# Optimization experiments

Hardware: AMD Instinct MI355X
Metric: run time of the kernel (lower is better)

## Reference

```python
import jax, jax.numpy as jnp
import numpy as np

N, E, IN_DIM, OUT_DIM, HEADS = 50000, 800000, 128, 64, 2
NEG_SLOPE = 0.2  # DGL GATConv default leaky_relu slope


def setup_inputs() -> dict:
    key = jax.random.key(0)
    ks = jax.random.split(key, 11)
    p = lambda k, shape: jax.random.normal(k, shape, jnp.float32) * 0.05
    return dict(
        feature=jax.random.normal(ks[0], (N, IN_DIM), jnp.float32),
        src=jax.random.randint(ks[1], (E,), 0, N, jnp.int32),
        dst=jax.random.randint(ks[2], (E,), 0, N, jnp.int32),
        W1=p(ks[3], (IN_DIM, HEADS * OUT_DIM)),
        al1=p(ks[4], (HEADS, OUT_DIM)),
        ar1=p(ks[5], (HEADS, OUT_DIM)),
        b1=p(ks[6], (HEADS * OUT_DIM,)),
        W2=p(ks[7], (HEADS * OUT_DIM, OUT_DIM)),
        al2=p(ks[8], (1, OUT_DIM)),
        ar2=p(ks[9], (1, OUT_DIM)),
        b2=p(ks[10], (OUT_DIM,)),
    )


def gat_conv(x, W, al, ar, b, src, dst, n_nodes):
    # DGL GATConv (eval mode): fc -> per-node attn halves -> edge leaky_relu
    # -> edge-softmax grouped by dst -> scatter-weighted sum -> + bias
    H, D = al.shape
    h = (x @ W).reshape(n_nodes, H, D)               # [N,H,D]
    el = jnp.einsum('nhd,hd->nh', h, al)             # [N,H]
    er = jnp.einsum('nhd,hd->nh', h, ar)             # [N,H]
    e = jax.nn.leaky_relu(el[src] + er[dst], NEG_SLOPE)  # [E,H]
    m = jax.ops.segment_max(e, dst, num_segments=n_nodes)
    m = jnp.where(jnp.isfinite(m), m, 0.0)           # guard isolated dst nodes
    ex = jnp.exp(e - m[dst])                         # [E,H]
    s = jax.ops.segment_sum(ex, dst, num_segments=n_nodes)
    alpha = ex / s[dst]                              # edge-softmax weights
    out = jax.ops.segment_sum(alpha[:, :, None] * h[src], dst,
                              num_segments=n_nodes)  # [N,H,D]
    return out + b.reshape(H, D)


def reference(feature, src, dst, W1, al1, ar1, b1, W2, al2, ar2, b2):
    h1 = jax.nn.elu(gat_conv(feature, W1, al1, ar1, b1, src, dst, N))  # [N,2,D]
    h2 = gat_conv(h1.reshape(N, -1), W2, al2, ar2, b2, src, dst, N)    # [N,1,D]
    return (h1.mean(axis=1) + h2[:, 0, :]) * 0.5
```

## Files before the change

### kernel.cpp

```cpp
#include <hip/hip_runtime.h>
#include <hip/hip_fp16.h>
#include <math.h>

#define NNODES 50000
#define NEDGES 800000
#define CSR_STRIDE 48
#define NBUCKET 256
#define CHUNK 196
#define BCAP 4096
#define EPB 4096

typedef short bf16x8 __attribute__((ext_vector_type(8)));
typedef float f32x4  __attribute__((ext_vector_type(4)));

__device__ __forceinline__ unsigned bfpack(float a, float b) {
    unsigned ua = __float_as_uint(a), ub = __float_as_uint(b);
    ua = (ua + 0x7fffu + ((ua >> 16) & 1u)) >> 16;
    ub = (ub + 0x7fffu + ((ub >> 16) & 1u)) >> 16;
    return ua | (ub << 16);
}
__device__ __forceinline__ unsigned h2pack(float a, float b) {
    __half2 h = __floats2half2_rn(a, b);
    return *(unsigned*)&h;
}
__device__ __forceinline__ float hlo(unsigned u) {
    union { unsigned u; __half2 h; } c; c.u = u; return __half2float(c.h.x);
}
__device__ __forceinline__ float hhi(unsigned u) {
    union { unsigned u; __half2 h; } c; c.u = u; return __half2float(c.h.y);
}

__global__ __launch_bounds__(256) void bucketA_kernel(
    const int* __restrict__ src, const int* __restrict__ dst,
    int* __restrict__ bcnt, unsigned* __restrict__ bbuf) {
    __shared__ int lcnt[NBUCKET];
    __shared__ int lcur[NBUCKET];
    const int tid = threadIdx.x;
    lcnt[tid] = 0;
    __syncthreads();
    const int e0 = blockIdx.x * EPB;
    int e1 = e0 + EPB; if (e1 > NEDGES) e1 = NEDGES;
    for (int e = e0 + tid; e < e1; e += 256)
        atomicAdd(&lcnt[dst[e] / CHUNK], 1);
    __syncthreads();
    int c = lcnt[tid];
    int base = 0;
    if (c > 0) base = atomicAdd(&bcnt[tid], c);
    lcur[tid] = tid * BCAP + base;
    __syncthreads();
    for (int e = e0 + tid; e < e1; e += 256) {
        int d = dst[e], s = src[e];
        int b = d / CHUNK;
        int pos = atomicAdd(&lcur[b], 1);
        if (pos < (b + 1) * BCAP)
            bbuf[pos] = ((unsigned)(d - b * CHUNK) << 16) | (unsigned)s;
    }
}

__global__ __launch_bounds__(256) void bucketB_kernel(
    const int* __restrict__ bcnt, const unsigned* __restrict__ bbuf,
    int* __restrict__ deg, unsigned short* __restrict__ pcsr) {
    const int b = blockIdx.x, tid = threadIdx.x;
    const int n0 = b * CHUNK;
    int ncnt = NNODES - n0; if (ncnt > CHUNK) ncnt = CHUNK;
    __shared__ int ldeg[CHUNK];
    __shared__ unsigned short lcsr[CHUNK * CSR_STRIDE];
    for (int i = tid; i < CHUNK; i += 256) ldeg[i] = 0;
    __syncthreads();
    int cnt = bcnt[b]; if (cnt > BCAP) cnt = BCAP;
    const unsigned* bb = bbuf + (size_t)b * BCAP;
    for (int i = tid; i < cnt; i += 256) {
        unsigned e = bb[i];
        int ln = e >> 16;
        int p = atomicAdd(&ldeg[ln], 1);
        if (p < CSR_STRIDE) lcsr[ln * CSR_STRIDE + p] = (unsigned short)(e & 0xffffu);
    }
    __syncthreads();
    for (int i = tid; i < ncnt; i += 256) deg[n0 + i] = ldeg[i];
    const int nv = ncnt * (CSR_STRIDE / 8);
    uint4* d4 = (uint4*)(pcsr + (size_t)n0 * CSR_STRIDE);
    const uint4* s4 = (const uint4*)lcsr;
    for (int i = tid; i < nv; i += 256) d4[i] = s4[i];
}

__global__ __launch_bounds__(256) void wt_kernel(const float* __restrict__ W1,
                                                 const float* __restrict__ W2,
                                                 unsigned* __restrict__ W1t,
                                                 unsigned* __restrict__ W2t) {
    int w = blockIdx.x * 256 + threadIdx.x;
    if (w < 8192) {
        int n = w >> 6, j = w & 63;
        W1t[w] = bfpack(W1[(2 * j) * 128 + n], W1[(2 * j + 1) * 128 + n]);
    } else {
        int w2 = w - 8192;
        int n = w2 >> 6, j = w2 & 63;
        W2t[w2] = bfpack(W2[(2 * j) * 64 + n], W2[(2 * j + 1) * 64 + n]);
    }
}

__global__ __launch_bounds__(256) void gemm1_kernel(
    const float* __restrict__ feat, const unsigned* __restrict__ Wt,
    const float* __restrict__ al, const float* __restrict__ ar,
    unsigned* __restrict__ h, float* __restrict__ el, float* __restrict__ er) {
    __shared__ unsigned Wb[128 * 68];
    __shared__ unsigned Ab[64 * 68];
    const int tid = threadIdx.x;
    const int n0  = blockIdx.x * 64;

#pragma unroll
    for (int i = 0; i < 8; ++i) {
        int id = i * 256 + tid;
        int n = id >> 4, c = (id & 15) * 4;
        *(uint4*)&Wb[n * 68 + c] = *(const uint4*)&Wt[n * 64 + c];
    }
#pragma unroll
    for (int i = 0; i < 8; ++i) {
        int f = i * 256 + tid;
        int m = f >> 5, cf = (f & 31) * 4;
        float4 v = make_float4(0.f, 0.f, 0.f, 0.f);
        if (n0 + m < NNODES)
            v = *(const float4*)&feat[(size_t)(n0 + m) * 128 + cf];
        uint2 p = {bfpack(v.x, v.y), bfpack(v.z, v.w)};
        *(uint2*)&Ab[m * 68 + cf / 2] = p;
    }
    __syncthreads();

    const int w  = tid >> 6;
    const int l  = tid & 63;
    const int ml = l & 15;
    const int q  = l >> 4;
    f32x4 acc[8];
#pragma unroll
    for (int t = 0; t < 8; ++t) acc[t] = (f32x4){0.f, 0.f, 0.f, 0.f};

#pragma unroll
    for (int kc = 0; kc < 4; ++kc) {
        const int kw = kc * 16 + q * 4;
        uint4 a4 = *(uint4*)&Ab[(16 * w + ml) * 68 + kw];
        bf16x8 af = *(bf16x8*)&a4;
#pragma unroll
        for (int t = 0; t < 8; ++t) {
            uint4 b4 = *(uint4*)&Wb[(t * 16 + ml) * 68 + kw];
            bf16x8 bf = *(bf16x8*)&b4;
            acc[t] = __builtin_amdgcn_mfma_f32_16x16x32_bf16(af, bf, acc[t], 0, 0, 0);
        }
    }

    float av[8], rv[8];
#pragma unroll
    for (int t = 0; t < 8; ++t) { av[t] = al[t * 16 + ml]; rv[t] = ar[t * 16 + ml]; }

#pragma unroll
    for (int r = 0; r < 4; ++r) {
        const int node = n0 + 16 * w + q * 4 + r;
        float e0 = 0.f, e1 = 0.f, f0 = 0.f, f1 = 0.f;
#pragma unroll
        for (int t = 0; t < 8; ++t) {
            float v = acc[t][r];
            if (t < 4) { e0 = fmaf(v, av[t], e0); f0 = fmaf(v, rv[t], f0); }
            else       { e1 = fmaf(v, av[t], e1); f1 = fmaf(v, rv[t], f1); }
            float pv = __shfl_xor(v, 1);
            if ((ml & 1) == 0 && node < NNODES)
                h[(size_t)node * 64 + t * 8 + (ml >> 1)] = h2pack(v, pv);
        }
#pragma unroll
        for (int mm = 1; mm <= 8; mm <<= 1) {
            e0 += __shfl_xor(e0, mm); e1 += __shfl_xor(e1, mm);
            f0 += __shfl_xor(f0, mm); f1 += __shfl_xor(f1, mm);
        }
        if (ml == 0 && node < NNODES) {
            el[node * 2 + 0] = e0; el[node * 2 + 1] = e1;
            er[node * 2 + 0] = f0; er[node * 2 + 1] = f1;
        }
    }
}

__global__ __launch_bounds__(256) void gemm2_kernel(
    const unsigned* __restrict__ h1b, const unsigned* __restrict__ Wt,
    const float* __restrict__ al, const float* __restrict__ ar,
    unsigned* __restrict__ h2, float* __restrict__ el, float* __restrict__ er) {
    __shared__ unsigned Wb[64 * 68];
    __shared__ unsigned Ab[64 * 68];
    const int tid = threadIdx.x;
    const int n0  = blockIdx.x * 64;

#pragma unroll
    for (int i = 0; i < 4; ++i) {
        int id = i * 256 + tid;
        int n = id >> 4, c = (id & 15) * 4;
        *(uint4*)&Wb[n * 68 + c] = *(const uint4*)&Wt[n * 64 + c];
    }
#pragma unroll
    for (int i = 0; i < 4; ++i) {
        int id = i * 256 + tid;
        int m = id >> 4, c = (id & 15) * 4;
        uint4 v = make_uint4(0u, 0u, 0u, 0u);
        if (n0 + m < NNODES)
            v = *(const uint4*)&h1b[(size_t)(n0 + m) * 64 + c];
        *(uint4*)&Ab[m * 68 + c] = v;
    }
    __syncthreads();

    const int w  = tid >> 6;
    const int l  = tid & 63;
    const int ml = l & 15;
    const int q  = l >> 4;
    f32x4 acc[4];
#pragma unroll
    for (int t = 0; t < 4; ++t) acc[t] = (f32x4){0.f, 0.f, 0.f, 0.f};

#pragma unroll
    for (int kc = 0; kc < 4; ++kc) {
        const int kw = kc * 16 + q * 4;
        uint4 a4 = *(uint4*)&Ab[(16 * w + ml) * 68 + kw];
        bf16x8 af = *(bf16x8*)&a4;
#pragma unroll
        for (int t = 0; t < 4; ++t) {
            uint4 b4 = *(uint4*)&Wb[(t * 16 + ml) * 68 + kw];
            bf16x8 bf = *(bf16x8*)&b4;
            acc[t] = __builtin_amdgcn_mfma_f32_16x16x32_bf16(af, bf, acc[t], 0, 0, 0);
        }
    }

    float av[4], rv[4];
#pragma unroll
    for (int t = 0; t < 4; ++t) { av[t] = al[t * 16 + ml]; rv[t] = ar[t * 16 + ml]; }

#pragma unroll
    for (int r = 0; r < 4; ++r) {
        const int node = n0 + 16 * w + q * 4 + r;
        float e0 = 0.f, f0 = 0.f;
#pragma unroll
        for (int t = 0; t < 4; ++t) {
            float v = acc[t][r];
            e0 = fmaf(v, av[t], e0);
            f0 = fmaf(v, rv[t], f0);
            float pv = __shfl_xor(v, 1);
            if ((ml & 1) == 0 && node < NNODES)
                h2[(size_t)node * 32 + t * 8 + (ml >> 1)] = h2pack(v, pv);
        }
#pragma unroll
        for (int mm = 1; mm <= 8; mm <<= 1) {
            e0 += __shfl_xor(e0, mm);
            f0 += __shfl_xor(f0, mm);
        }
        if (ml == 0 && node < NNODES) { el[node] = e0; er[node] = f0; }
    }
}

#define FMA8(hv, A)                                              \
    a0r = fmaf(hlo(hv.x), A, a0r); a1r = fmaf(hhi(hv.x), A, a1r); \
    a2r = fmaf(hlo(hv.y), A, a2r); a3r = fmaf(hhi(hv.y), A, a3r); \
    a4r = fmaf(hlo(hv.z), A, a4r); a5r = fmaf(hhi(hv.z), A, a5r); \
    a6r = fmaf(hlo(hv.w), A, a6r); a7r = fmaf(hhi(hv.w), A, a7r);

__global__ __launch_bounds__(256) void aggregate1_kernel(
    const int* __restrict__ degv,
    const unsigned short* __restrict__ csr_src,
    const float* __restrict__ el, const float* __restrict__ er,
    const unsigned* __restrict__ hh, const float* __restrict__ bias,
    unsigned* __restrict__ h1b, float* __restrict__ hm) {
    const int wid  = (blockIdx.x * 256 + threadIdx.x) >> 6;
    const int lane = threadIdx.x & 63;
    const int hl   = lane & 31;
    const int lb   = lane & 32;
    const int node = wid * 2 + (lane >> 5);
    if (node >= NNODES) return;
    const int row = node * CSR_STRIDE;
    int deg = degv[node];
    deg = deg < CSR_STRIDE ? deg : CSR_STRIDE;
    const float er0 = er[node * 2 + 0];
    const float er1 = er[node * 2 + 1];

    const int  q2    = hl >> 4;
    const int  ql    = hl & 15;
    const bool h1sel = (ql >= 8);
    const unsigned* __restrict__ hq = hh + 4 * ql;

    int s_reg = 0;
    if (hl < deg) s_reg = (int)csr_src[row + hl];

    uint4 hv[8];
#pragma unroll
    for (int j = 0; j < 8; ++j) {
        int s = __shfl(s_reg, lb + 2 * j + q2);
        hv[j] = *(const uint4*)(hq + (size_t)s * 64);
    }
    int dm  = deg < 32 ? deg : 32;
    int dmW = max(dm, __shfl_xor(dm, 32));
    const bool doB = dmW > 16;
    uint4 hw[8];
    if (doB) {
#pragma unroll
        for (int j = 0; j < 8; ++j) {
            int s = __shfl(s_reg, lb + 16 + 2 * j + q2);
            hw[j] = *(const uint4*)(hq + (size_t)s * 64);
        }
    }

    float2 e2 = *(const float2*)&el[s_reg * 2];
    float a = e2.x + er0; a = a > 0.f ? a : 0.2f * a;
    float b = e2.y + er1; b = b > 0.f ? b : 0.2f * b;
    float v0 = (hl < deg) ? a : -1e30f;
    float v1 = (hl < deg) ? b : -1e30f;
    float m0 = v0, m1 = v1;
    for (int i = 32 + hl; i < deg; i += 32) {
        int s = (int)csr_src[row + i];
        float2 ee = *(const float2*)&el[s * 2];
        float aa = ee.x + er0; aa = aa > 0.f ? aa : 0.2f * aa;
        float bb = ee.y + er1; bb = bb > 0.f ? bb : 0.2f * bb;
        m0 = fmaxf(m0, aa); m1 = fmaxf(m1, bb);
    }
#pragma unroll
    for (int off = 16; off > 0; off >>= 1) {
        m0 = fmaxf(m0, __shfl_xor(m0, off));
        m1 = fmaxf(m1, __shfl_xor(m1, off));
    }
    float p0 = __expf(v0 - m0);
    float p1 = __expf(v1 - m1);
    float ssum0 = p0, ssum1 = p1;
    for (int i = 32 + hl; i < deg; i += 32) {
        int s = (int)csr_src[row + i];
        float2 ee = *(const float2*)&el[s * 2];
        float aa = ee.x + er0; aa = aa > 0.f ? aa : 0.2f * aa;
        float bb = ee.y + er1; bb = bb > 0.f ? bb : 0.2f * bb;
        ssum0 += __expf(aa - m0); ssum1 += __expf(bb - m1);
    }
#pragma unroll
    for (int off = 16; off > 0; off >>= 1) {
        ssum0 += __shfl_xor(ssum0, off);
        ssum1 += __shfl_xor(ssum1, off);
    }

    float a0r = 0.f, a1r = 0.f, a2r = 0.f, a3r = 0.f;
    float a4r = 0.f, a5r = 0.f, a6r = 0.f, a7r = 0.f;
#pragma unroll
    for (int j = 0; j < 8; ++j) {
        const int sl_ = lb + 2 * j + q2;
        float x = __shfl(p0, sl_);
        float y = __shfl(p1, sl_);
        float A = h1sel ? y : x;
        FMA8(hv[j], A)
    }
    if (doB) {
#pragma unroll
        for (int j = 0; j < 8; ++j) {
            const int sl_ = lb + 16 + 2 * j + q2;
            float x = __shfl(p0, sl_);
            float y = __shfl(p1, sl_);
            float A = h1sel ? y : x;
            FMA8(hw[j], A)
        }
    }
    for (int i2 = 32; i2 < deg; i2 += 2) {
        int eidx = i2 + q2;
        if (eidx < deg) {
            int s = (int)csr_src[row + eidx];
            float2 ee = *(const float2*)&el[s * 2];
            float aa = ee.x + er0; aa = aa > 0.f ? aa : 0.2f * aa;
            float bb = ee.y + er1; bb = bb > 0.f ? bb : 0.2f * bb;
            float alpha = h1sel ? __expf(bb - m1) : __expf(aa - m0);
            uint4 h4 = *(const uint4*)(hq + (size_t)s * 64);
            FMA8(h4, alpha)
        }
    }
    a0r += __shfl_xor(a0r, 16);  a1r += __shfl_xor(a1r, 16);
    a2r += __shfl_xor(a2r, 16);  a3r += __shfl_xor(a3r, 16);
    a4r += __shfl_xor(a4r, 16);  a5r += __shfl_xor(a5r, 16);
    a6r += __shfl_xor(a6r, 16);  a7r += __shfl_xor(a7r, 16);

    const float ssum = h1sel ? ssum1 : ssum0;
    const float inv  = (deg > 0) ? 1.f / ssum : 0.f;
    float4 b0 = *(const float4*)&bias[8 * ql];
    float4 b1 = *(const float4*)&bias[8 * ql + 4];
    float o0 = fmaf(a0r, inv, b0.x), o1 = fmaf(a1r, inv, b0.y);
    float o2 = fmaf(a2r, inv, b0.z), o3 = fmaf(a3r, inv, b0.w);
    float o4 = fmaf(a4r, inv, b1.x), o5 = fmaf(a5r, inv, b1.y);
    float o6 = fmaf(a6r, inv, b1.z), o7 = fmaf(a7r, inv, b1.w);
    o0 = o0 > 0.f ? o0 : (__expf(o0) - 1.f);
    o1 = o1 > 0.f ? o1 : (__expf(o1) - 1.f);
    o2 = o2 > 0.f ? o2 : (__expf(o2) - 1.f);
    o3 = o3 > 0.f ? o3 : (__expf(o3) - 1.f);
    o4 = o4 > 0.f ? o4 : (__expf(o4) - 1.f);
    o5 = o5 > 0.f ? o5 : (__expf(o5) - 1.f);
    o6 = o6 > 0.f ? o6 : (__expf(o6) - 1.f);
    o7 = o7 > 0.f ? o7 : (__expf(o7) - 1.f);

    if (hl < 16) {
        uint4 pk;
        pk.x = bfpack(o0, o1); pk.y = bfpack(o2, o3);
        pk.z = bfpack(o4, o5); pk.w = bfpack(o6, o7);
        *(uint4*)&h1b[(size_t)node * 64 + 4 * ql] = pk;
    }
    float n0_ = 0.5f * (o0 + __shfl_xor(o0, 8));
    float n1_ = 0.5f * (o1 + __shfl_xor(o1, 8));
    float n2_ = 0.5f * (o2 + __shfl_xor(o2, 8));
    float n3_ = 0.5f * (o3 + __shfl_xor(o3, 8));
    float n4_ = 0.5f * (o4 + __shfl_xor(o4, 8));
    float n5_ = 0.5f * (o5 + __shfl_xor(o5, 8));
    float n6_ = 0.5f * (o6 + __shfl_xor(o6, 8));
    float n7_ = 0.5f * (o7 + __shfl_xor(o7, 8));
    if (hl < 8) {
        *(float4*)&hm[(size_t)node * 64 + 8 * hl]     = make_float4(n0_, n1_, n2_, n3_);
        *(float4*)&hm[(size_t)node * 64 + 8 * hl + 4] = make_float4(n4_, n5_, n6_, n7_);
    }
}

#define FMA4(hv, P)                                            \
    ax = fmaf(hlo(hv.x), P, ax); ay = fmaf(hhi(hv.x), P, ay);  \
    az = fmaf(hlo(hv.y), P, az); aw = fmaf(hhi(hv.y), P, aw);

__global__ __launch_bounds__(256) void aggregate2_kernel(
    const int* __restrict__ degv,
    const unsigned short* __restrict__ csr_src,
    const float* __restrict__ el, const float* __restrict__ er,
    const unsigned* __restrict__ hh, const float* __restrict__ bias,
    const float* __restrict__ hm, float* __restrict__ outp) {
    const int wid  = (blockIdx.x * 256 + threadIdx.x) >> 6;
    const int lane = threadIdx.x & 63;
    const int hl   = lane & 31;
    const int lb   = lane & 32;
    const int node = wid * 2 + (lane >> 5);
    if (node >= NNODES) return;
    const int row = node * CSR_STRIDE;
    int deg = degv[node];
    deg = deg < CSR_STRIDE ? deg : CSR_STRIDE;
    const float erd = er[node];

    const int s2 = hl >> 4;
    const int sl = hl & 15;
    const unsigned* __restrict__ hq = hh + 2 * sl;

    int s_reg = 0;
    if (hl < deg) s_reg = (int)csr_src[row + hl];

    uint2 hv[8];
#pragma unroll
    for (int j = 0; j < 8; ++j) {
        int s = __shfl(s_reg, lb + 2 * j + s2);
        hv[j] = *(const uint2*)(hq + (size_t)s * 32);
    }
    int dm  = deg < 32 ? deg : 32;
    int dmW = max(dm, __shfl_xor(dm, 32));
    const bool doB = dmW > 16;
    uint2 hw[8];
    if (doB) {
#pragma unroll
        for (int j = 0; j < 8; ++j) {
            int s = __shfl(s_reg, lb + 16 + 2 * j + s2);
            hw[j] = *(const uint2*)(hq + (size_t)s * 32);
        }
    }

    float v = el[s_reg] + erd;
    v = v > 0.f ? v : 0.2f * v;
    float v_reg = (hl < deg) ? v : -1e30f;
    float m = v_reg;
    for (int i = 32 + hl; i < deg; i += 32) {
        int s = (int)csr_src[row + i];
        float vv = el[s] + erd;
        vv = vv > 0.f ? vv : 0.2f * vv;
        m = fmaxf(m, vv);
    }
#pragma unroll
    for (int off = 16; off > 0; off >>= 1) m = fmaxf(m, __shfl_xor(m, off));

    float p_reg = __expf(v_reg - m);
    float ssum = p_reg;
    for (int i = 32 + hl; i < deg; i += 32) {
        int s = (int)csr_src[row + i];
        float vv = el[s] + erd;
        vv = vv > 0.f ? vv : 0.2f * vv;
        ssum += __expf(vv - m);
    }
#pragma unroll
    for (int off = 16; off > 0; off >>= 1) ssum += __shfl_xor(ssum, off);

    float ax = 0.f, ay = 0.f, az = 0.f, aw = 0.f;
#pragma unroll
    for (int j = 0; j < 8; ++j) {
        const int sl_ = lb + 2 * j + s2;
        float p = __shfl(p_reg, sl_);
        FMA4(hv[j], p)
    }
    if (doB) {
#pragma unroll
        for (int j = 0; j < 8; ++j) {
            const int sl_ = lb + 16 + 2 * j + s2;
            float p = __shfl(p_reg, sl_);
            FMA4(hw[j], p)
        }
    }
    for (int i2 = 32; i2 < deg; i2 += 2) {
        int eidx = i2 + s2;
        if (eidx < deg) {
            int s = (int)csr_src[row + eidx];
            float vv = el[s] + erd;
            vv = vv > 0.f ? vv : 0.2f * vv;
            float p = __expf(vv - m);
            uint2 h2v = *(const uint2*)(hq + (size_t)s * 32);
            FMA4(h2v, p)
        }
    }
    ax += __shfl_xor(ax, 16);  ay += __shfl_xor(ay, 16);
    az += __shfl_xor(az, 16);  aw += __shfl_xor(aw, 16);

    if (sl == hl) {
        float inv = (deg > 0) ? 1.f / ssum : 0.f;
        float4 hmv = *(const float4*)&hm[(size_t)node * 64 + 4 * sl];
        float4 bb  = *(const float4*)&bias[4 * sl];
        float o0 = (hmv.x + fmaf(ax, inv, bb.x)) * 0.5f;
        float o1 = (hmv.y + fmaf(ay, inv, bb.y)) * 0.5f;
        float o2 = (hmv.z + fmaf(az, inv, bb.z)) * 0.5f;
        float o3 = (hmv.w + fmaf(aw, inv, bb.w)) * 0.5f;
        *(float4*)&outp[(size_t)node * 64 + 4 * sl] = make_float4(o0, o1, o2, o3);
    }
}


extern "C" void kernel_launch(void* const* d_in, const int* in_sizes, int n_in,
                              void* d_out, int out_size, void* d_ws, size_t ws_size,
                              hipStream_t stream) {
    const float* feat = (const float*)d_in[0];
    const int*   src  = (const int*)d_in[1];
    const int*   dst  = (const int*)d_in[2];
    const float* W1   = (const float*)d_in[3];
    const float* al1  = (const float*)d_in[4];
    const float* ar1  = (const float*)d_in[5];
    const float* b1   = (const float*)d_in[6];
    const float* W2   = (const float*)d_in[7];
    const float* al2  = (const float*)d_in[8];
    const float* ar2  = (const float*)d_in[9];
    const float* b2   = (const float*)d_in[10];
    float* out = (float*)d_out;

    int*            bcnt   = (int*)d_ws;
    int*            ideg   = bcnt + NBUCKET;
    unsigned*       iw1t   = (unsigned*)(ideg + NNODES);
    unsigned*       iw2t   = iw1t + 8192;
    unsigned short* pcsr   = (unsigned short*)(iw2t + 4096);
    unsigned*       gH1    = (unsigned*)(pcsr + (size_t)NNODES * CSR_STRIDE);
    unsigned*       bbuf   = gH1;
    unsigned*       gH2    = gH1;
    unsigned*       h1b    = gH1 + (size_t)NNODES * 64;
    float*          hmean  = (float*)(h1b + (size_t)NNODES * 64);
    float*          fEl1   = hmean + (size_t)NNODES * 64;
    float*          fEr1   = fEl1 + (size_t)NNODES * 2;
    float*          fEl2   = fEr1 + (size_t)NNODES * 2;
    float*          fEr2   = fEl2 + (size_t)NNODES;

    hipMemsetAsync(bcnt, 0, NBUCKET * sizeof(int), stream);
    bucketA_kernel<<<(NEDGES + EPB - 1) / EPB, 256, 0, stream>>>(src, dst, bcnt, bbuf);
    bucketB_kernel<<<NBUCKET, 256, 0, stream>>>(bcnt, bbuf, ideg, pcsr);
    wt_kernel<<<48, 256, 0, stream>>>(W1, W2, iw1t, iw2t);

    gemm1_kernel<<<(NNODES + 63) / 64, 256, 0, stream>>>(feat, iw1t, al1, ar1,
                                                         gH1, fEl1, fEr1);
    aggregate1_kernel<<<(NNODES / 2 + 3) / 4, 256, 0, stream>>>(
        ideg, pcsr, fEl1, fEr1, gH1, b1, h1b, hmean);

    gemm2_kernel<<<(NNODES + 63) / 64, 256, 0, stream>>>(h1b, iw2t, al2, ar2,
                                                         gH2, fEl2, fEr2);
    aggregate2_kernel<<<(NNODES / 2 + 3) / 4, 256, 0, stream>>>(
        ideg, pcsr, fEl2, fEr2, gH2, b2, hmean, out);
}
```

Baseline: 207.3 us.

## Map 16 lanes per node in aggregation kernels and fold bucket-count memset into wt_kernel

The aggregation kernels now assign 16 lanes per destination node (4 nodes per wavefront) instead of 32. Each lane handles a full 8-feature slice, which removes the cross-half reduction shuffles and the serial tail loop. Edges come in up to three fixed 16-edge batches, so each edge's score is computed once and kept in registers rather than recomputed across the max, sum and accumulate passes. The hipMemsetAsync on the bucket counters becomes a store inside wt_kernel, which now launches first, saving one stream operation. The trade-offs are higher register pressure from the 16-element gather arrays, possible occupancy loss, and more divergence between nodes of different degree in the same wave.

Result: no change. 207.9 us (+0.3%).

```diff
diff --git a/kernel.cpp b/kernel.cpp
--- a/kernel.cpp
+++ b/kernel.cpp
@@ -86,7 +86,9 @@
 __global__ __launch_bounds__(256) void wt_kernel(const float* __restrict__ W1,
                                                  const float* __restrict__ W2,
                                                  unsigned* __restrict__ W1t,
-                                                 unsigned* __restrict__ W2t) {
+                                                 unsigned* __restrict__ W2t,
+                                                 int* __restrict__ bcnt) {
+    if (blockIdx.x == 0) bcnt[threadIdx.x] = 0;
     int w = blockIdx.x * 256 + threadIdx.x;
     if (w < 8192) {
         int n = w >> 6, j = w & 63;
@@ -262,72 +264,64 @@
     unsigned* __restrict__ h1b, float* __restrict__ hm) {
     const int wid  = (blockIdx.x * 256 + threadIdx.x) >> 6;
     const int lane = threadIdx.x & 63;
-    const int hl   = lane & 31;
-    const int lb   = lane & 32;
-    const int node = wid * 2 + (lane >> 5);
+    const int g    = lane >> 4;
+    const int l16  = lane & 15;
+    const int gb   = g * 16;
+    const int node = wid * 4 + g;
     if (node >= NNODES) return;
     const int row = node * CSR_STRIDE;
     int deg = degv[node];
     deg = deg < CSR_STRIDE ? deg : CSR_STRIDE;
     const float er0 = er[node * 2 + 0];
     const float er1 = er[node * 2 + 1];
-
-    const int  q2    = hl >> 4;
-    const int  ql    = hl & 15;
-    const bool h1sel = (ql >= 8);
-    const unsigned* __restrict__ hq = hh + 4 * ql;
-
-    int s_reg = 0;
-    if (hl < deg) s_reg = (int)csr_src[row + hl];
-
-    uint4 hv[8];
-#pragma unroll
-    for (int j = 0; j < 8; ++j) {
-        int s = __shfl(s_reg, lb + 2 * j + q2);
+    const bool hsel = (l16 >= 8);
+    const unsigned* __restrict__ hq = hh + 4 * l16;
+
+    int s0 = 0;
+    if (l16 < deg) s0 = (int)csr_src[row + l16];
+
+    uint4 hv[16];
+#pragma unroll
+    for (int j = 0; j < 16; ++j) {
+        int s = __shfl(s0, gb + j);
         hv[j] = *(const uint4*)(hq + (size_t)s * 64);
     }
-    int dm  = deg < 32 ? deg : 32;
-    int dmW = max(dm, __shfl_xor(dm, 32));
-    const bool doB = dmW > 16;
-    uint4 hw[8];
-    if (doB) {
-#pragma unroll
-        for (int j = 0; j < 8; ++j) {
-            int s = __shfl(s_reg, lb + 16 + 2 * j + q2);
-            hw[j] = *(const uint4*)(hq + (size_t)s * 64);
-        }
-    }
-
-    float2 e2 = *(const float2*)&el[s_reg * 2];
+
+    float2 e2 = *(const float2*)&el[s0 * 2];
     float a = e2.x + er0; a = a > 0.f ? a : 0.2f * a;
     float b = e2.y + er1; b = b > 0.f ? b : 0.2f * b;
-    float v0 = (hl < deg) ? a : -1e30f;
-    float v1 = (hl < deg) ? b : -1e30f;
+    float v0 = (l16 < deg) ? a : -1e30f;
+    float v1 = (l16 < deg) ? b : -1e30f;
     float m0 = v0, m1 = v1;
-    for (int i = 32 + hl; i < deg; i += 32) {
-        int s = (int)csr_src[row + i];
-        float2 ee = *(const float2*)&el[s * 2];
-        float aa = ee.x + er0; aa = aa > 0.f ? aa : 0.2f * aa;
-        float bb = ee.y + er1; bb = bb > 0.f ? bb : 0.2f * bb;
-        m0 = fmaxf(m0, aa); m1 = fmaxf(m1, bb);
-    }
-#pragma unroll
-    for (int off = 16; off > 0; off >>= 1) {
+    int   s1 = 0, s2 = 0;
+    float va1 = -1e30f, vb1 = -1e30f, va2 = -1e30f, vb2 = -1e30f;
+    if (deg > 16) {
+        if (16 + l16 < deg) {
+            s1 = (int)csr_src[row + 16 + l16];
+            float2 ee = *(const float2*)&el[s1 * 2];
+            float aa = ee.x + er0; va1 = aa > 0.f ? aa : 0.2f * aa;
+            float bb = ee.y + er1; vb1 = bb > 0.f ? bb : 0.2f * bb;
+            m0 = fmaxf(m0, va1); m1 = fmaxf(m1, vb1);
+        }
+        if (32 + l16 < deg) {
+            s2 = (int)csr_src[row + 32 + l16];
+            float2 ee = *(const float2*)&el[s2 * 2];
+            float aa = ee.x + er0; va2 = aa > 0.f ? aa : 0.2f * aa;
+            float bb = ee.y + er1; vb2 = bb > 0.f ? bb : 0.2f * bb;
+            m0 = fmaxf(m0, va2); m1 = fmaxf(m1, vb2);
+        }
+    }
+#pragma unroll
+    for (int off = 8; off > 0; off >>= 1) {
         m0 = fmaxf(m0, __shfl_xor(m0, off));
         m1 = fmaxf(m1, __shfl_xor(m1, off));
     }
-    float p0 = __expf(v0 - m0);
-    float p1 = __expf(v1 - m1);
-    float ssum0 = p0, ssum1 = p1;
-    for (int i = 32 + hl; i < deg; i += 32) {
-        int s = (int)csr_src[row + i];
-        float2 ee = *(const float2*)&el[s * 2];
-        float aa = ee.x + er0; aa = aa > 0.f ? aa : 0.2f * aa;
-        float bb = ee.y + er1; bb = bb > 0.f ? bb : 0.2f * bb;
-        ssum0 += __expf(aa - m0); ssum1 += __expf(bb - m1);
-    }
-#pragma unroll
-    for (int off = 16; off > 0; off >>= 1) {
+    float p0 = __expf(v0 - m0),  p1 = __expf(v1 - m1);
+    float q0 = __expf(va1 - m0), q1 = __expf(vb1 - m1);
+    float r0 = __expf(va2 - m0), r1 = __expf(vb2 - m1);
+    float ssum0 = p0 + q0 + r0, ssum1 = p1 + q1 + r1;
+#pragma unroll
+    for (int off = 8; off > 0; off >>= 1) {
         ssum0 += __shfl_xor(ssum0, off);
         ssum1 += __shfl_xor(ssum1, off);
     }
@@ -335,44 +329,47 @@
     float a0r = 0.f, a1r = 0.f, a2r = 0.f, a3r = 0.f;
     float a4r = 0.f, a5r = 0.f, a6r = 0.f, a7r = 0.f;
 #pragma unroll
-    for (int j = 0; j < 8; ++j) {
-        const int sl_ = lb + 2 * j + q2;
-        float x = __shfl(p0, sl_);
-        float y = __shfl(p1, sl_);
-        float A = h1sel ? y : x;
+    for (int j = 0; j < 16; ++j) {
+        float x = __shfl(p0, gb + j);
+        float y = __shfl(p1, gb + j);
+        float A = hsel ? y : x;
         FMA8(hv[j], A)
     }
-    if (doB) {
-#pragma unroll
-        for (int j = 0; j < 8; ++j) {
-            const int sl_ = lb + 16 + 2 * j + q2;
-            float x = __shfl(p0, sl_);
-            float y = __shfl(p1, sl_);
-            float A = h1sel ? y : x;
+    if (deg > 16) {
+        uint4 hw[16];
+#pragma unroll
+        for (int j = 0; j < 16; ++j) {
+            int s = __shfl(s1, gb + j);
+            hw[j] = *(const uint4*)(hq + (size_t)s * 64);
+        }
+#pragma unroll
+        for (int j = 0; j < 16; ++j) {
+            float x = __shfl(q0, gb + j);
+            float y = __shfl(q1, gb + j);
+            float A = hsel ? y : x;
             FMA8(hw[j], A)
         }
     }
-    for (int i2 = 32; i2 < deg; i2 += 2) {
-        int eidx = i2 + q2;
-        if (eidx < deg) {
-            int s = (int)csr_src[row + eidx];
-            float2 ee = *(const float2*)&el[s * 2];
-            float aa = ee.x + er0; aa = aa > 0.f ? aa : 0.2f * aa;
-            float bb = ee.y + er1; bb = bb > 0.f ? bb : 0.2f * bb;
-            float alpha = h1sel ? __expf(bb - m1) : __expf(aa - m0);
-            uint4 h4 = *(const uint4*)(hq + (size_t)s * 64);
-            FMA8(h4, alpha)
-        }
-    }
-    a0r += __shfl_xor(a0r, 16);  a1r += __shfl_xor(a1r, 16);
-    a2r += __shfl_xor(a2r, 16);  a3r += __shfl_xor(a3r, 16);
-    a4r += __shfl_xor(a4r, 16);  a5r += __shfl_xor(a5r, 16);
-    a6r += __shfl_xor(a6r, 16);  a7r += __shfl_xor(a7r, 16);
-
-    const float ssum = h1sel ? ssum1 : ssum0;
+    if (deg > 32) {
+        uint4 hz[16];
+#pragma unroll
+        for (int j = 0; j < 16; ++j) {
+            int s = __shfl(s2, gb + j);
+            hz[j] = *(const uint4*)(hq + (size_t)s * 64);
+        }
+#pragma unroll
+        for (int j = 0; j < 16; ++j) {
+            float x = __shfl(r0, gb + j);
+            float y = __shfl(r1, gb + j);
+            float A = hsel ? y : x;
+            FMA8(hz[j], A)
+        }
+    }
+
+    const float ssum = hsel ? ssum1 : ssum0;
     const float inv  = (deg > 0) ? 1.f / ssum : 0.f;
-    float4 b0 = *(const float4*)&bias[8 * ql];
-    float4 b1 = *(const float4*)&bias[8 * ql + 4];
+    float4 b0 = *(const float4*)&bias[8 * l16];
+    float4 b1 = *(const float4*)&bias[8 * l16 + 4];
     float o0 = fmaf(a0r, inv, b0.x), o1 = fmaf(a1r, inv, b0.y);
     float o2 = fmaf(a2r, inv, b0.z), o3 = fmaf(a3r, inv, b0.w);
     float o4 = fmaf(a4r, inv, b1.x), o5 = fmaf(a5r, inv, b1.y);
@@ -386,12 +383,11 @@
     o6 = o6 > 0.f ? o6 : (__expf(o6) - 1.f);
     o7 = o7 > 0.f ? o7 : (__expf(o7) - 1.f);
 
-    if (hl < 16) {
-        uint4 pk;
-        pk.x = bfpack(o0, o1); pk.y = bfpack(o2, o3);
-        pk.z = bfpack(o4, o5); pk.w = bfpack(o6, o7);
-        *(uint4*)&h1b[(size_t)node * 64 + 4 * ql] = pk;
-    }
+    uint4 pk;
+    pk.x = bfpack(o0, o1); pk.y = bfpack(o2, o3);
+    pk.z = bfpack(o4, o5); pk.w = bfpack(o6, o7);
+    *(uint4*)&h1b[(size_t)node * 64 + 4 * l16] = pk;
+
     float n0_ = 0.5f * (o0 + __shfl_xor(o0, 8));
     float n1_ = 0.5f * (o1 + __shfl_xor(o1, 8));
     float n2_ = 0.5f * (o2 + __shfl_xor(o2, 8));
@@ -400,9 +396,9 @@
     float n5_ = 0.5f * (o5 + __shfl_xor(o5, 8));
     float n6_ = 0.5f * (o6 + __shfl_xor(o6, 8));
     float n7_ = 0.5f * (o7 + __shfl_xor(o7, 8));
-    if (hl < 8) {
-        *(float4*)&hm[(size_t)node * 64 + 8 * hl]     = make_float4(n0_, n1_, n2_, n3_);
-        *(float4*)&hm[(size_t)node * 64 + 8 * hl + 4] = make_float4(n4_, n5_, n6_, n7_);
+    if (l16 < 8) {
+        *(float4*)&hm[(size_t)node * 64 + 8 * l16]     = make_float4(n0_, n1_, n2_, n3_);
+        *(float4*)&hm[(size_t)node * 64 + 8 * l16 + 4] = make_float4(n4_, n5_, n6_, n7_);
     }
 }
 
@@ -418,103 +414,97 @@
     const float* __restrict__ hm, float* __restrict__ outp) {
     const int wid  = (blockIdx.x * 256 + threadIdx.x) >> 6;
     const int lane = threadIdx.x & 63;
-    const int hl   = lane & 31;
-    const int lb   = lane & 32;
-    const int node = wid * 2 + (lane >> 5);
+    const int g    = lane >> 4;
+    const int l16  = lane & 15;
+    const int gb   = g * 16;
+    const int node = wid * 4 + g;
     if (node >= NNODES) return;
     const int row = node * CSR_STRIDE;
     int deg = degv[node];
     deg = deg < CSR_STRIDE ? deg : CSR_STRIDE;
     const float erd = er[node];
-
-    const int s2 = hl >> 4;
-    const int sl = hl & 15;
-    const unsigned* __restrict__ hq = hh + 2 * sl;
-
-    int s_reg = 0;
-    if (hl < deg) s_reg = (int)csr_src[row + hl];
-
-    uint2 hv[8];
-#pragma unroll
-    for (int j = 0; j < 8; ++j) {
-        int s = __shfl(s_reg, lb + 2 * j + s2);
+    const unsigned* __restrict__ hq = hh + 2 * l16;
+
+    int s0 = 0;
+    if (l16 < deg) s0 = (int)csr_src[row + l16];
+
+    uint2 hv[16];
+#pragma unroll
+    for (int j = 0; j < 16; ++j) {
+        int s = __shfl(s0, gb + j);
         hv[j] = *(const uint2*)(hq + (size_t)s * 32);
     }
-    int dm  = deg < 32 ? deg : 32;
-    int dmW = max(dm, __shfl_xor(dm, 32));
-    const bool doB = dmW > 16;
-    uint2 hw[8];
-    if (doB) {
-#pragma unroll
-        for (int j = 0; j < 8; ++j) {
-            int s = __shfl(s_reg, lb + 16 + 2 * j + s2);
+
+    float v = el[s0] + erd;
+    v = v > 0.f ? v : 0.2f * v;
+    float v0 = (l16 < deg) ? v : -1e30f;
+    float m = v0;
+    int   s1 = 0, s2 = 0;
+    float va1 = -1e30f, va2 = -1e30f;
+    if (deg > 16) {
+        if (16 + l16 < deg) {
+            s1 = (int)csr_src[row + 16 + l16];
+            float vv = el[s1] + erd;
+            va1 = vv > 0.f ? vv : 0.2f * vv;
+            m = fmaxf(m, va1);
+        }
+        if (32 + l16 < deg) {
+            s2 = (int)csr_src[row + 32 + l16];
+            float vv = el[s2] + erd;
+            va2 = vv > 0.f ? vv : 0.2f * vv;
+            m = fmaxf(m, va2);
+        }
+    }
+#pragma unroll
+    for (int off = 8; off > 0; off >>= 1) m = fmaxf(m, __shfl_xor(m, off));
+    float p0 = __expf(v0 - m);
+    float q0 = __expf(va1 - m);
+    float r0 = __expf(va2 - m);
+    float ssum = p0 + q0 + r0;
+#pragma unroll
+    for (int off = 8; off > 0; off >>= 1) ssum += __shfl_xor(ssum, off);
+
+    float ax = 0.f, ay = 0.f, az = 0.f, aw = 0.f;
+#pragma unroll
+    for (int j = 0; j < 16; ++j) {
+        float p = __shfl(p0, gb + j);
+        FMA4(hv[j], p)
+    }
+    if (deg > 16) {
+        uint2 hw[16];
+#pragma unroll
+        for (int j = 0; j < 16; ++j) {
+            int s = __shfl(s1, gb + j);
             hw[j] = *(const uint2*)(hq + (size_t)s * 32);
         }
-    }
-
-    float v = el[s_reg] + erd;
-    v = v > 0.f ? v : 0.2f * v;
-    float v_reg = (hl < deg) ? v : -1e30f;
-    float m = v_reg;
-    for (int i = 32 + hl; i < deg; i += 32) {
-        int s = (int)csr_src[row + i];
-        float vv = el[s] + erd;
-        vv = vv > 0.f ? vv : 0.2f * vv;
-        m = fmaxf(m, vv);
-    }
-#pragma unroll
-    for (int off = 16; off > 0; off >>= 1) m = fmaxf(m, __shfl_xor(m, off));
-
-    float p_reg = __expf(v_reg - m);
-    float ssum = p_reg;
-    for (int i = 32 + hl; i < deg; i += 32) {
-        int s = (int)csr_src[row + i];
-        float vv = el[s] + erd;
-        vv = vv > 0.f ? vv : 0.2f * vv;
-        ssum += __expf(vv - m);
-    }
-#pragma unroll
-    for (int off = 16; off > 0; off >>= 1) ssum += __shfl_xor(ssum, off);
-
-    float ax = 0.f, ay = 0.f, az = 0.f, aw = 0.f;
-#pragma unroll
-    for (int j = 0; j < 8; ++j) {
-        const int sl_ = lb + 2 * j + s2;
-        float p = __shfl(p_reg, sl_);
-        FMA4(hv[j], p)
-    }
-    if (doB) {
-#pragma unroll
-        for (int j = 0; j < 8; ++j) {
-            const int sl_ = lb + 16 + 2 * j + s2;
-            float p = __shfl(p_reg, sl_);
+#pragma unroll
+        for (int j = 0; j < 16; ++j) {
+            float p = __shfl(q0, gb + j);
             FMA4(hw[j], p)
         }
     }
-    for (int i2 = 32; i2 < deg; i2 += 2) {
-        int eidx = i2 + s2;
-        if (eidx < deg) {
-            int s = (int)csr_src[row + eidx];
-            float vv = el[s] + erd;
-            vv = vv > 0.f ? vv : 0.2f * vv;
-            float p = __expf(vv - m);
-            uint2 h2v = *(const uint2*)(hq + (size_t)s * 32);
-            FMA4(h2v, p)
-        }
-    }
-    ax += __shfl_xor(ax, 16);  ay += __shfl_xor(ay, 16);
-    az += __shfl_xor(az, 16);  aw += __shfl_xor(aw, 16);
-
-    if (sl == hl) {
-        float inv = (deg > 0) ? 1.f / ssum : 0.f;
-        float4 hmv = *(const float4*)&hm[(size_t)node * 64 + 4 * sl];
-        float4 bb  = *(const float4*)&bias[4 * sl];
-        float o0 = (hmv.x + fmaf(ax, inv, bb.x)) * 0.5f;
-        float o1 = (hmv.y + fmaf(ay, inv, bb.y)) * 0.5f;
-        float o2 = (hmv.z + fmaf(az, inv, bb.z)) * 0.5f;
-        float o3 = (hmv.w + fmaf(aw, inv, bb.w)) * 0.5f;
-        *(float4*)&outp[(size_t)node * 64 + 4 * sl] = make_float4(o0, o1, o2, o3);
-    }
+    if (deg > 32) {
+        uint2 hz[16];
+#pragma unroll
+        for (int j = 0; j < 16; ++j) {
+            int s = __shfl(s2, gb + j);
+            hz[j] = *(const uint2*)(hq + (size_t)s * 32);
+        }
+#pragma unroll
+        for (int j = 0; j < 16; ++j) {
+            float p = __shfl(r0, gb + j);
+            FMA4(hz[j], p)
+        }
+    }
+
+    float inv = (deg > 0) ? 1.f / ssum : 0.f;
+    float4 hmv = *(const float4*)&hm[(size_t)node * 64 + 4 * l16];
+    float4 bb  = *(const float4*)&bias[4 * l16];
+    float o0 = (hmv.x + fmaf(ax, inv, bb.x)) * 0.5f;
+    float o1 = (hmv.y + fmaf(ay, inv, bb.y)) * 0.5f;
+    float o2 = (hmv.z + fmaf(az, inv, bb.z)) * 0.5f;
+    float o3 = (hmv.w + fmaf(aw, inv, bb.w)) * 0.5f;
+    *(float4*)&outp[(size_t)node * 64 + 4 * l16] = make_float4(o0, o1, o2, o3);
 }
 
 
@@ -549,18 +539,17 @@
     float*          fEl2   = fEr1 + (size_t)NNODES * 2;
     float*          fEr2   = fEl2 + (size_t)NNODES;
 
-    hipMemsetAsync(bcnt, 0, NBUCKET * sizeof(int), stream);
+    wt_kernel<<<48, 256, 0, stream>>>(W1, W2, iw1t, iw2t, bcnt);
     bucketA_kernel<<<(NEDGES + EPB - 1) / EPB, 256, 0, stream>>>(src, dst, bcnt, bbuf);
     bucketB_kernel<<<NBUCKET, 256, 0, stream>>>(bcnt, bbuf, ideg, pcsr);
-    wt_kernel<<<48, 256, 0, stream>>>(W1, W2, iw1t, iw2t);
 
     gemm1_kernel<<<(NNODES + 63) / 64, 256, 0, stream>>>(feat, iw1t, al1, ar1,
                                                          gH1, fEl1, fEr1);
-    aggregate1_kernel<<<(NNODES / 2 + 3) / 4, 256, 0, stream>>>(
+    aggregate1_kernel<<<(NNODES + 15) / 16, 256, 0, stream>>>(
         ideg, pcsr, fEl1, fEr1, gH1, b1, h1b, hmean);
 
     gemm2_kernel<<<(NNODES + 63) / 64, 256, 0, stream>>>(h1b, iw2t, al2, ar2,
                                                          gH2, fEl2, fEr2);
-    aggregate2_kernel<<<(NNODES / 2 + 3) / 4, 256, 0, stream>>>(
+    aggregate2_kernel<<<(NNODES + 15) / 16, 256, 0, stream>>>(
         ideg, pcsr, fEl2, fEr2, gH2, b2, hmean, out);
 }
```
